# Kernel tuning notes

Measured on AMD Instinct MI355X. Metric: run time of the kernel, lower is better.

Reference implementation:

```python
import jax, jax.numpy as jnp
import numpy as np

N = 4096            # num nodes
D = 256             # feature dim
NUM_SUPER_NODES = 6
THRESHOLD = 0.0
EPS = 1e-10
DENSITY = 0.02      # pre-symmetrization edge density


def setup_inputs() -> dict:
    key = jax.random.key(0)
    kx, ka = jax.random.split(key)
    X = jax.random.normal(kx, (N, D), dtype=jnp.float32)
    U = jax.random.uniform(ka, (N, N), dtype=jnp.float32)
    A = (U < DENSITY).astype(jnp.float32)
    A = jnp.maximum(A, A.T)                      # symmetric 0/1 adjacency
    A = A * (1.0 - jnp.eye(N, dtype=jnp.float32))  # no self-loops
    return {"X": X, "A": A}


def _greedy_labels(sim_np, n, num_super, threshold):
    """Sequential greedy union-find merge over pairs sorted by similarity.
    Matches torch: stable descending sort on sim only; merge until
    n - merged <= num_super; relabel roots in first-occurrence order.
    Inherently sequential/data-dependent -> done in numpy on concrete values
    (the torch original also detaches via .item())."""
    iu, ju = np.triu_indices(n, k=1)
    sims = sim_np[iu, ju]
    keep = sims >= threshold
    iu, ju, sims = iu[keep], ju[keep], sims[keep]
    order = np.argsort(-sims, kind="stable")     # stable desc == list.sort(reverse=True)
    parent = np.arange(n)

    def find(i):
        while parent[i] != i:
            parent[i] = parent[parent[i]]        # path halving
            i = parent[i]
        return i

    merged = 0
    for k in order:
        pi, pj = find(int(iu[k])), find(int(ju[k]))
        if pi != pj:
            parent[pj] = pi
            merged += 1
            if n - merged <= num_super:
                break
    mapping = {}
    labels = np.empty(n, dtype=np.int64)
    nl = 0
    for i in range(n):
        r = find(i)
        if r not in mapping:
            mapping[r] = nl
            nl += 1
        labels[i] = mapping[r]
    return labels, nl


def _build_P(A):
    """Vectorized pairwise Jaccard (replaces O(n^2) python loop) + greedy merge."""
    n = A.shape[0]
    A_bin = (A > 0).astype(jnp.float32)
    deg = A_bin.sum(axis=1)                      # |N(i)|
    inter = A_bin @ A_bin.T                      # [n,n] pairwise |Ni & Nj|
    union = deg[:, None] + deg[None, :] - inter  # |Ni | Nj|
    sim = jnp.where(union > 0, inter / jnp.maximum(union, 1.0), 0.0)
    labels, m = _greedy_labels(np.asarray(sim), n, NUM_SUPER_NODES, THRESHOLD)
    P_prime = jax.nn.one_hot(jnp.asarray(labels), m, dtype=jnp.float32)  # [n, m]
    sizes = P_prime.sum(axis=0)
    return P_prime / jnp.sqrt(sizes + EPS)[None, :]   # P = P' @ diag(1/sqrt(sizes+eps))


def reference(X, A):
    P = _build_P(A)                               # [n, m], m == NUM_SUPER_NODES
    X_coarse = P.T @ X                            # [m, D]
    A_coarse = P.T @ A @ P                        # [m, m]
    return (X_coarse, A_coarse, P)
```

## Files before the change

### kernel.cpp

```cpp
#include <hip/hip_runtime.h>

typedef unsigned long long u64;
typedef unsigned short u16;

#define NN 4096
#define NCH 64
#define NSUP 6

__global__ __launch_bounds__(256) void k_packdeg(const float* __restrict__ A,
                                                 u64* __restrict__ bits,
                                                 u16* __restrict__ deg,
                                                 float* out, int out_n,
                                                 int* comp, int* ncomp, int* mstcnt) {
  int t = threadIdx.x;
  int w = t >> 6, lane = t & 63;
  int row = blockIdx.x * 4 + w;
  const float* rp = A + (size_t)row * NN;
  u64 my = 0;
  int dsum = 0;
#pragma unroll 8
  for (int k = 0; k < 64; ++k) {
    float v = rp[k * 64 + lane];
    u64 m = __ballot(v > 0.0f);
    dsum += __popcll(m);
    if (lane == k) my = m;
  }
  bits[(size_t)row * NCH + lane] = my;
  if (lane == 0) deg[row] = (u16)dsum;
  int g = blockIdx.x * 256 + t;
  if (g < out_n) out[g] = 0.0f;
  if (g < NN) comp[g] = g;
  if (g == 0) { *ncomp = NN; *mstcnt = 0; }
}

__global__ __launch_bounds__(256) void k_inter(const u64* __restrict__ bits,
                                               u16* __restrict__ inter) {
  __shared__ ulonglong2 L[2][64 * 8];
  int b = blockIdx.x;
  int by = (int)((129.0f - sqrtf(16641.0f - 8.0f * (float)b)) * 0.5f) - 1;
  if (by < 0) by = 0;
#define CUM(y) (64 * (y) - ((y) * ((y) - 1)) / 2)
  while (by < 63 && CUM(by + 1) <= b) ++by;
  while (CUM(by) > b) --by;
  int bx = by + (b - CUM(by));
#undef CUM
  int i0 = by * 64, j0 = bx * 64;
  int t = threadIdx.x;
  int tx = t & 15, ty = t >> 4;
  int swA = ty & 7, swB = tx & 7;
  int slotL = t & 7, rowL = t >> 3;
  int sw0 = (rowL >> 2) & 7, sw1 = ((rowL + 32) >> 2) & 7;
  int acc[4][4] = {};
  for (int st = 0; st < 4; ++st) {
    __syncthreads();
    {
      const ulonglong2* gi0 = reinterpret_cast<const ulonglong2*>(bits + (size_t)(i0 + rowL) * NCH);
      const ulonglong2* gi1 = reinterpret_cast<const ulonglong2*>(bits + (size_t)(i0 + rowL + 32) * NCH);
      const ulonglong2* gj0 = reinterpret_cast<const ulonglong2*>(bits + (size_t)(j0 + rowL) * NCH);
      const ulonglong2* gj1 = reinterpret_cast<const ulonglong2*>(bits + (size_t)(j0 + rowL + 32) * NCH);
      L[0][rowL * 8 + (slotL ^ sw0)] = gi0[st * 8 + slotL];
      L[0][(rowL + 32) * 8 + (slotL ^ sw1)] = gi1[st * 8 + slotL];
      L[1][rowL * 8 + (slotL ^ sw0)] = gj0[st * 8 + slotL];
      L[1][(rowL + 32) * 8 + (slotL ^ sw1)] = gj1[st * 8 + slotL];
    }
    __syncthreads();
    for (int s = 0; s < 8; ++s) {
      ulonglong2 av[4], bv[4];
#pragma unroll
      for (int a = 0; a < 4; ++a) av[a] = L[0][(ty * 4 + a) * 8 + (s ^ swA)];
#pragma unroll
      for (int c = 0; c < 4; ++c) bv[c] = L[1][(tx * 4 + c) * 8 + (s ^ swB)];
#pragma unroll
      for (int a = 0; a < 4; ++a)
#pragma unroll
        for (int c = 0; c < 4; ++c)
          acc[a][c] += __popcll(av[a].x & bv[c].x) + __popcll(av[a].y & bv[c].y);
    }
  }
#pragma unroll
  for (int a = 0; a < 4; ++a) {
    int i = i0 + ty * 4 + a;
    ushort4 wv;
    wv.x = (u16)acc[a][0]; wv.y = (u16)acc[a][1];
    wv.z = (u16)acc[a][2]; wv.w = (u16)acc[a][3];
    *reinterpret_cast<ushort4*>(inter + (size_t)i * NN + j0 + tx * 4) = wv;
  }
  if (bx != by) {
#pragma unroll
    for (int c = 0; c < 4; ++c) {
      int j = j0 + tx * 4 + c;
      ushort4 wv;
      wv.x = (u16)acc[0][c]; wv.y = (u16)acc[1][c];
      wv.z = (u16)acc[2][c]; wv.w = (u16)acc[3][c];
      *reinterpret_cast<ushort4*>(inter + (size_t)j * NN + i0 + ty * 4) = wv;
    }
  }
}

__global__ __launch_bounds__(256) void k_scan(const u16* __restrict__ inter,
                                              const u16* __restrict__ deg,
                                              const int* __restrict__ comp,
                                              const int* __restrict__ ncomp,
                                              u64* __restrict__ nkey,
                                              int* __restrict__ nu) {
  if (*ncomp <= 1) return;
  __shared__ u16 comp_s[NN];
  __shared__ u16 deg_s[NN];
  int t = threadIdx.x;
  for (int i = t; i < NN / 8; i += 256) {
    int4 ca = reinterpret_cast<const int4*>(comp)[i * 2];
    int4 cb = reinterpret_cast<const int4*>(comp)[i * 2 + 1];
    uint4 pk;
    pk.x = (unsigned)ca.x | ((unsigned)ca.y << 16);
    pk.y = (unsigned)ca.z | ((unsigned)ca.w << 16);
    pk.z = (unsigned)cb.x | ((unsigned)cb.y << 16);
    pk.w = (unsigned)cb.z | ((unsigned)cb.w << 16);
    reinterpret_cast<uint4*>(comp_s)[i] = pk;
    reinterpret_cast<uint4*>(deg_s)[i] = reinterpret_cast<const uint4*>(deg)[i];
  }
  __syncthreads();
  int w = t >> 6, lane = t & 63;
  int v = blockIdx.x * 4 + w;
  int cv = (int)comp_s[v];
  int dv = (int)deg_s[v];
  const u16* row = inter + (size_t)v * NN;
  u64 key = 0;
  for (int it = 0; it < 8; ++it) {
    int ub = it * 512 + lane * 8;
    uint4 pv = *reinterpret_cast<const uint4*>(row + ub);
    uint4 dg = reinterpret_cast<const uint4*>(deg_s)[ub >> 3];
    uint4 cs = reinterpret_cast<const uint4*>(comp_s)[ub >> 3];
    unsigned pw[4] = { pv.x, pv.y, pv.z, pv.w };
    unsigned dw[4] = { dg.x, dg.y, dg.z, dg.w };
    unsigned cw[4] = { cs.x, cs.y, cs.z, cs.w };
#pragma unroll
    for (int k = 0; k < 8; ++k) {
      int iv = (int)((pw[k >> 1] >> ((k & 1) * 16)) & 0xFFFF);
      int du = (int)((dw[k >> 1] >> ((k & 1) * 16)) & 0xFFFF);
      int cu = (int)((cw[k >> 1] >> ((k & 1) * 16)) & 0xFFFF);
      int un = dv + du - iv;
      float s = (un > 0) ? ((float)iv / (float)un) : 0.0f;
      unsigned sb = __float_as_uint(s);
      u64 kk = (cu != cv)
                   ? (((u64)sb << 32) | (u64)(0xFFFFFFFFu - (unsigned)(ub + k)))
                   : 0ull;
      if (kk > key) key = kk;
    }
  }
#pragma unroll
  for (int off = 32; off > 0; off >>= 1) {
    unsigned lo = (unsigned)key, hi = (unsigned)(key >> 32);
    unsigned olo = __shfl_xor(lo, off, 64), ohi = __shfl_xor(hi, off, 64);
    u64 o = ((u64)ohi << 32) | (u64)olo;
    if (o > key) key = o;
  }
  if (lane == 0) {
    u64 pk = 0; int u = -1;
    if (key != 0ull) {
      unsigned simb = (unsigned)(key >> 32);
      u = (int)(0xFFFFFFFFu - (unsigned)(key & 0xFFFFFFFFull));
      int i = v < u ? v : u, j = v < u ? u : v;
      unsigned idx = (unsigned)i * (unsigned)(2 * NN - i - 1) / 2u + (unsigned)(j - i - 1);
      pk = ((u64)simb << 24) | (u64)(0xFFFFFFu - idx);
    }
    nkey[v] = pk; nu[v] = u;
  }
}

__global__ __launch_bounds__(1024) void k_merge(const u64* __restrict__ nkey,
                                                const int* __restrict__ nu,
                                                int* comp, int* ncomp, int* mstcnt,
                                                u64* mkey, int* mi, int* mj,
                                                int* labels_g, float* invs_g, float* out) {
  if (*ncomp <= 1) return;
  __shared__ int parent_s[NN];
  __shared__ u64 cbest_s[NN];
  __shared__ unsigned char mk_s[NN];
  __shared__ int roots[16];
  __shared__ int rcnt, cnt_s, chg_s, changed;
  __shared__ int szs[8];
  __shared__ float ivs[8];
  int t = threadIdx.x;
  for (int c = t; c < NN; c += 1024) { parent_s[c] = c; cbest_s[c] = 0ull; }
  __syncthreads();
  for (int v = t; v < NN; v += 1024) {
    u64 k = nkey[v];
    if (k) atomicMax(&cbest_s[comp[v]], k);
  }
  __syncthreads();
  for (int v = t; v < NN; v += 1024) {
    u64 k = nkey[v];
    if (!k) continue;
    int c = comp[v];
    if (k == cbest_s[c]) {
      int u = nu[v];
      int cu = comp[u];
      bool mutual = (cbest_s[cu] == k);
      if (!mutual || v < u) {
        int slot = atomicAdd(mstcnt, 1);
        if (slot < 4352) { mkey[slot] = k; mi[slot] = v; mj[slot] = u; }
      }
      parent_s[c] = cu;
    }
  }
  __syncthreads();
  for (int c = t; c < NN; c += 1024) {
    int pc = parent_s[c];
    if (parent_s[pc] == c && c < pc) parent_s[c] = c;
  }
  __syncthreads();
  for (int it = 0; it < 13; ++it) {
    if (t == 0) chg_s = 0;
    __syncthreads();
    for (int c = t; c < NN; c += 1024) {
      int p1 = parent_s[c], p2 = parent_s[p1];
      if (p1 != p2) { parent_s[c] = p2; chg_s = 1; }
    }
    __syncthreads();
    if (!chg_s) break;
  }
  for (int c = t; c < NN; c += 1024) mk_s[c] = 0;
  if (t == 0) cnt_s = 0;
  __syncthreads();
  for (int v = t; v < NN; v += 1024) {
    int nc = parent_s[comp[v]];
    comp[v] = nc;
    mk_s[nc] = 1;
  }
  __syncthreads();
  int lc = 0;
  for (int c = t; c < NN; c += 1024) lc += mk_s[c];
  atomicAdd(&cnt_s, lc);
  __syncthreads();
  if (t == 0) *ncomp = cnt_s;
  __syncthreads();
  if (cnt_s != 1) return;
  int* rr = reinterpret_cast<int*>(cbest_s);
  u64* rk = cbest_s + 2048;
  int* rs = reinterpret_cast<int*>(cbest_s + 3072);
  int nm = *mstcnt;
  if (nm < 0) nm = 0;
  if (nm > 4352) nm = 4352;
  for (int v = t; v < NN; v += 1024) parent_s[v] = v;
  for (int pass = 0; pass < NSUP - 1; ++pass) {
    u64 bk = ~0ull; int bsel = -1;
    for (int e = t; e < nm; e += 1024) { u64 k = mkey[e]; if (k < bk) { bk = k; bsel = e; } }
    rk[t] = bk; rs[t] = bsel;
    __syncthreads();
    for (int s = 512; s > 0; s >>= 1) {
      if (t < s && rk[t + s] < rk[t]) { rk[t] = rk[t + s]; rs[t] = rs[t + s]; }
      __syncthreads();
    }
    if (t == 0 && rs[0] >= 0) mkey[rs[0]] = ~0ull;
    __syncthreads();
  }
  for (int round = 0; round < 64; ++round) {
    if (t == 0) changed = 0;
    __syncthreads();
    for (int e = t; e < nm; e += 1024) {
      if (mkey[e] == ~0ull) continue;
      int a = parent_s[mi[e]], b = parent_s[mj[e]];
      if (a == b) continue;
      int m = a < b ? a : b, M = a < b ? b : a;
      int old = atomicMin(&parent_s[M], m);
      if (old > m) changed = 1;
    }
    __syncthreads();
    for (int rep = 0; rep < 3; ++rep) {
      for (int v = t; v < NN; v += 1024) parent_s[v] = parent_s[parent_s[v]];
      __syncthreads();
    }
    int ch = changed;
    __syncthreads();
    if (!ch) break;
  }
  for (int rep = 0; rep < 13; ++rep) {
    for (int v = t; v < NN; v += 1024) parent_s[v] = parent_s[parent_s[v]];
    __syncthreads();
  }
  if (t == 0) rcnt = 0;
  __syncthreads();
  for (int v = t; v < NN; v += 1024)
    if (parent_s[v] == v) { int s = atomicAdd(&rcnt, 1); if (s < 16) roots[s] = v; }
  __syncthreads();
  if (t == 0) {
    int c = rcnt > 16 ? 16 : rcnt;
    for (int a = 1; a < c; ++a) {
      int x = roots[a]; int b2 = a - 1;
      while (b2 >= 0 && roots[b2] > x) { roots[b2 + 1] = roots[b2]; --b2; }
      roots[b2 + 1] = x;
    }
  }
  if (t < 8) szs[t] = 0;
  __syncthreads();
  if (t < rcnt && t < 16) rr[roots[t]] = t;
  __syncthreads();
  for (int v = t; v < NN; v += 1024) {
    int lab = rr[parent_s[v]];
    labels_g[v] = lab;
    atomicAdd(&szs[lab], 1);
  }
  __syncthreads();
  if (t < rcnt && t < 8) {
    float iv = 1.0f / sqrtf((float)szs[t] + 1e-10f);
    ivs[t] = iv; invs_g[t] = iv;
  }
  __syncthreads();
  for (int v = t; v < NN; v += 1024) {
    int lab = rr[parent_s[v]];
    float* base = out + 1572 + v * 6;
#pragma unroll
    for (int b2 = 0; b2 < 6; ++b2) base[b2] = (b2 == lab) ? ivs[lab] : 0.0f;
  }
}

__global__ __launch_bounds__(256) void k_coarse(const float* __restrict__ X,
                                                const u64* __restrict__ bits,
                                                const int* __restrict__ labels,
                                                const float* __restrict__ invs,
                                                float* out) {
  int t = threadIdx.x;
  if (blockIdx.x < 64) {
    __shared__ float acc[6][256];
    __shared__ int labs[64];
    __shared__ float ivl[64];
#pragma unroll
    for (int m = 0; m < 6; ++m) acc[m][t] = 0.0f;
    if (t < 64) { int v = blockIdx.x * 64 + t; int l = labels[v]; labs[t] = l; ivl[t] = invs[l]; }
    __syncthreads();
    int v0 = blockIdx.x * 64;
    for (int r = 0; r < 64; ++r) {
      float x = X[(size_t)(v0 + r) * 256 + t];
      acc[labs[r]][t] += ivl[r] * x;
    }
    __syncthreads();
#pragma unroll
    for (int m = 0; m < 6; ++m) atomicAdd(&out[m * 256 + t], acc[m][t]);
  } else {
    __shared__ unsigned char labs8[NN];
    __shared__ float accA[36];
    __shared__ float ivsl[8];
    for (int v = t; v < NN; v += 256) labs8[v] = (unsigned char)labels[v];
    if (t < 36) accA[t] = 0.0f;
    if (t < 6) ivsl[t] = invs[t];
    __syncthreads();
    int i = (blockIdx.x - 64) * 256 + t;
    u64 cnt = 0;
    const u64* row = bits + (size_t)i * NCH;
    for (int c = 0; c < NCH; ++c) {
      u64 wm = row[c];
      while (wm) {
        int j = (c << 6) + __builtin_ctzll(wm);
        wm &= wm - 1;
        cnt += 1ull << (labs8[j] * 10);
      }
    }
    int li = labs8[i];
    float fi = ivsl[li];
#pragma unroll
    for (int b = 0; b < 6; ++b) {
      float cb = (float)((cnt >> (b * 10)) & 1023ull);
      if (cb != 0.0f) atomicAdd(&accA[li * 6 + b], fi * ivsl[b] * cb);
    }
    __syncthreads();
    if (t < 36) atomicAdd(&out[1536 + t], accA[t]);
  }
}

extern "C" void kernel_launch(void* const* d_in, const int* in_sizes, int n_in,
                              void* d_out, int out_size, void* d_ws, size_t ws_size,
                              hipStream_t stream) {
  const float* X = (const float*)d_in[0];
  const float* A = (const float*)d_in[1];
  float* out = (float*)d_out;

  char* wp = (char*)d_ws;
  size_t off = 0;
#define WALLOC(ty, name, count) \
  ty* name = (ty*)(wp + off);   \
  off += (((size_t)(count) * sizeof(ty)) + 255) & ~(size_t)255;
  WALLOC(u64, bits, (size_t)NN * NCH)
  WALLOC(u16, inter, (size_t)NN * NN)
  WALLOC(u16, deg, NN)
  WALLOC(int, comp, NN)
  WALLOC(u64, nkey, NN)
  WALLOC(int, nu, NN)
  WALLOC(u64, mkey, 4352)
  WALLOC(int, mi, 4352)
  WALLOC(int, mj, 4352)
  WALLOC(int, labels, NN)
  WALLOC(float, invs, 8)
  WALLOC(int, ncomp, 1)
  WALLOC(int, mstcnt, 1)
#undef WALLOC
  if (off > ws_size) return;

  k_packdeg<<<NN / 4, 256, 0, stream>>>(A, bits, deg, out, out_size, comp, ncomp, mstcnt);
  k_inter<<<2080, 256, 0, stream>>>(bits, inter);
  for (int ph = 0; ph < 12; ++ph) {
    k_scan<<<NN / 4, 256, 0, stream>>>(inter, deg, comp, ncomp, nkey, nu);
    k_merge<<<1, 1024, 0, stream>>>(nkey, nu, comp, ncomp, mstcnt, mkey, mi, mj,
                                    labels, invs, out);
  }
  k_coarse<<<80, 256, 0, stream>>>(X, bits, labels, invs, out);
}
```

Before: 381.9 us.

## Fuse scan and merge into one kernel using last-block completion counter

Merges the per-phase scan kernel and the single-block merge kernel into one launch. The last block to finish, detected with an atomic done counter, performs the Boruvka merge using global cbest and 16-bit shared parent arrays. This removes 12 kernel launches and the serial 1024-thread launch gap each phase, at the cost of running the merge with only 256 threads. The inter kernel is also reworked to load 16 chunks per stage with a different LDS swizzle, halving the number of staging rounds.

```diff
diff --git a/kernel.cpp b/kernel.cpp
--- a/kernel.cpp
+++ b/kernel.cpp
@@ -6,12 +6,14 @@
 #define NN 4096
 #define NCH 64
 #define NSUP 6
+#define NPB 1024
 
 __global__ __launch_bounds__(256) void k_packdeg(const float* __restrict__ A,
                                                  u64* __restrict__ bits,
                                                  u16* __restrict__ deg,
                                                  float* out, int out_n,
-                                                 int* comp, int* ncomp, int* mstcnt) {
+                                                 int* comp, int* ncomp, int* mstcnt,
+                                                 u64* cbest, unsigned* done) {
   int t = threadIdx.x;
   int w = t >> 6, lane = t & 63;
   int row = blockIdx.x * 4 + w;
@@ -29,13 +31,14 @@
   if (lane == 0) deg[row] = (u16)dsum;
   int g = blockIdx.x * 256 + t;
   if (g < out_n) out[g] = 0.0f;
-  if (g < NN) comp[g] = g;
+  if (g < NN) { comp[g] = g; cbest[g] = 0ull; }
+  if (g < 16) done[g] = 0u;
   if (g == 0) { *ncomp = NN; *mstcnt = 0; }
 }
 
 __global__ __launch_bounds__(256) void k_inter(const u64* __restrict__ bits,
                                                u16* __restrict__ inter) {
-  __shared__ ulonglong2 L[2][64 * 8];
+  __shared__ ulonglong2 L[2][64 * 16];
   int b = blockIdx.x;
   int by = (int)((129.0f - sqrtf(16641.0f - 8.0f * (float)b)) * 0.5f) - 1;
   if (by < 0) by = 0;
@@ -47,34 +50,37 @@
   int i0 = by * 64, j0 = bx * 64;
   int t = threadIdx.x;
   int tx = t & 15, ty = t >> 4;
-  int swA = ty & 7, swB = tx & 7;
-  int slotL = t & 7, rowL = t >> 3;
-  int sw0 = (rowL >> 2) & 7, sw1 = ((rowL + 32) >> 2) & 7;
+  int rowA[4], swA[4], rowB[4], swB[4];
+#pragma unroll
+  for (int a = 0; a < 4; ++a) {
+    rowA[a] = ty * 4 + a; swA[a] = (rowA[a] ^ (rowA[a] >> 2)) & 7;
+    rowB[a] = tx * 4 + a; swB[a] = (rowB[a] ^ (rowB[a] >> 2)) & 7;
+  }
+  int cuL = t & 15, rg = t >> 4;
   int acc[4][4] = {};
-  for (int st = 0; st < 4; ++st) {
-    __syncthreads();
-    {
-      const ulonglong2* gi0 = reinterpret_cast<const ulonglong2*>(bits + (size_t)(i0 + rowL) * NCH);
-      const ulonglong2* gi1 = reinterpret_cast<const ulonglong2*>(bits + (size_t)(i0 + rowL + 32) * NCH);
-      const ulonglong2* gj0 = reinterpret_cast<const ulonglong2*>(bits + (size_t)(j0 + rowL) * NCH);
-      const ulonglong2* gj1 = reinterpret_cast<const ulonglong2*>(bits + (size_t)(j0 + rowL + 32) * NCH);
-      L[0][rowL * 8 + (slotL ^ sw0)] = gi0[st * 8 + slotL];
-      L[0][(rowL + 32) * 8 + (slotL ^ sw1)] = gi1[st * 8 + slotL];
-      L[1][rowL * 8 + (slotL ^ sw0)] = gj0[st * 8 + slotL];
-      L[1][(rowL + 32) * 8 + (slotL ^ sw1)] = gj1[st * 8 + slotL];
-    }
-    __syncthreads();
-    for (int s = 0; s < 8; ++s) {
+  for (int st = 0; st < 2; ++st) {
+    __syncthreads();
+#pragma unroll
+    for (int rr = 0; rr < 4; ++rr) {
+      int row = rg * 4 + rr;
+      int sw = (row ^ (row >> 2)) & 7;
+      L[0][row * 16 + (cuL ^ sw)] =
+          reinterpret_cast<const ulonglong2*>(bits + (size_t)(i0 + row) * NCH)[st * 16 + cuL];
+      L[1][row * 16 + (cuL ^ sw)] =
+          reinterpret_cast<const ulonglong2*>(bits + (size_t)(j0 + row) * NCH)[st * 16 + cuL];
+    }
+    __syncthreads();
+    for (int cu = 0; cu < 16; ++cu) {
       ulonglong2 av[4], bv[4];
 #pragma unroll
-      for (int a = 0; a < 4; ++a) av[a] = L[0][(ty * 4 + a) * 8 + (s ^ swA)];
-#pragma unroll
-      for (int c = 0; c < 4; ++c) bv[c] = L[1][(tx * 4 + c) * 8 + (s ^ swB)];
+      for (int a = 0; a < 4; ++a) av[a] = L[0][rowA[a] * 16 + (cu ^ swA[a])];
+#pragma unroll
+      for (int b2 = 0; b2 < 4; ++b2) bv[b2] = L[1][rowB[b2] * 16 + (cu ^ swB[b2])];
 #pragma unroll
       for (int a = 0; a < 4; ++a)
 #pragma unroll
-        for (int c = 0; c < 4; ++c)
-          acc[a][c] += __popcll(av[a].x & bv[c].x) + __popcll(av[a].y & bv[c].y);
+        for (int b2 = 0; b2 < 4; ++b2)
+          acc[a][b2] += __popcll(av[a].x & bv[b2].x) + __popcll(av[a].y & bv[b2].y);
     }
   }
 #pragma unroll
@@ -87,25 +93,32 @@
   }
   if (bx != by) {
 #pragma unroll
-    for (int c = 0; c < 4; ++c) {
-      int j = j0 + tx * 4 + c;
+    for (int b2 = 0; b2 < 4; ++b2) {
+      int j = j0 + tx * 4 + b2;
       ushort4 wv;
-      wv.x = (u16)acc[0][c]; wv.y = (u16)acc[1][c];
-      wv.z = (u16)acc[2][c]; wv.w = (u16)acc[3][c];
+      wv.x = (u16)acc[0][b2]; wv.y = (u16)acc[1][b2];
+      wv.z = (u16)acc[2][b2]; wv.w = (u16)acc[3][b2];
       *reinterpret_cast<ushort4*>(inter + (size_t)j * NN + i0 + ty * 4) = wv;
     }
   }
 }
 
-__global__ __launch_bounds__(256) void k_scan(const u16* __restrict__ inter,
-                                              const u16* __restrict__ deg,
-                                              const int* __restrict__ comp,
-                                              const int* __restrict__ ncomp,
-                                              u64* __restrict__ nkey,
-                                              int* __restrict__ nu) {
+__global__ __launch_bounds__(256) void k_phase(const u16* __restrict__ inter,
+                                               const u16* __restrict__ deg,
+                                               int* comp, int* ncomp, int* mstcnt,
+                                               u64* __restrict__ nkey, int* __restrict__ nu,
+                                               u64* mkey, int* mi, int* mj,
+                                               u64* cbest, unsigned* done, int ph,
+                                               int* labels_g, float* invs_g, float* out) {
   if (*ncomp <= 1) return;
   __shared__ u16 comp_s[NN];
   __shared__ u16 deg_s[NN];
+  __shared__ u64 rk[256];
+  __shared__ int rs[256];
+  __shared__ int roots[16];
+  __shared__ int rcnt, cnt_s, chg_s, changed, amLast;
+  __shared__ int szs[8];
+  __shared__ float ivs[8];
   int t = threadIdx.x;
   for (int i = t; i < NN / 8; i += 256) {
     int4 ca = reinterpret_cast<const int4*>(comp)[i * 2];
@@ -119,135 +132,136 @@
     reinterpret_cast<uint4*>(deg_s)[i] = reinterpret_cast<const uint4*>(deg)[i];
   }
   __syncthreads();
-  int w = t >> 6, lane = t & 63;
-  int v = blockIdx.x * 4 + w;
-  int cv = (int)comp_s[v];
-  int dv = (int)deg_s[v];
-  const u16* row = inter + (size_t)v * NN;
-  u64 key = 0;
-  for (int it = 0; it < 8; ++it) {
-    int ub = it * 512 + lane * 8;
-    uint4 pv = *reinterpret_cast<const uint4*>(row + ub);
-    uint4 dg = reinterpret_cast<const uint4*>(deg_s)[ub >> 3];
-    uint4 cs = reinterpret_cast<const uint4*>(comp_s)[ub >> 3];
-    unsigned pw[4] = { pv.x, pv.y, pv.z, pv.w };
-    unsigned dw[4] = { dg.x, dg.y, dg.z, dg.w };
-    unsigned cw[4] = { cs.x, cs.y, cs.z, cs.w };
-#pragma unroll
-    for (int k = 0; k < 8; ++k) {
-      int iv = (int)((pw[k >> 1] >> ((k & 1) * 16)) & 0xFFFF);
-      int du = (int)((dw[k >> 1] >> ((k & 1) * 16)) & 0xFFFF);
-      int cu = (int)((cw[k >> 1] >> ((k & 1) * 16)) & 0xFFFF);
-      int un = dv + du - iv;
-      float s = (un > 0) ? ((float)iv / (float)un) : 0.0f;
-      unsigned sb = __float_as_uint(s);
-      u64 kk = (cu != cv)
-                   ? (((u64)sb << 32) | (u64)(0xFFFFFFFFu - (unsigned)(ub + k)))
-                   : 0ull;
-      if (kk > key) key = kk;
-    }
-  }
-#pragma unroll
-  for (int off = 32; off > 0; off >>= 1) {
-    unsigned lo = (unsigned)key, hi = (unsigned)(key >> 32);
-    unsigned olo = __shfl_xor(lo, off, 64), ohi = __shfl_xor(hi, off, 64);
-    u64 o = ((u64)ohi << 32) | (u64)olo;
-    if (o > key) key = o;
-  }
-  if (lane == 0) {
-    u64 pk = 0; int u = -1;
-    if (key != 0ull) {
-      unsigned simb = (unsigned)(key >> 32);
-      u = (int)(0xFFFFFFFFu - (unsigned)(key & 0xFFFFFFFFull));
-      int i = v < u ? v : u, j = v < u ? u : v;
-      unsigned idx = (unsigned)i * (unsigned)(2 * NN - i - 1) / 2u + (unsigned)(j - i - 1);
-      pk = ((u64)simb << 24) | (u64)(0xFFFFFFu - idx);
-    }
-    nkey[v] = pk; nu[v] = u;
-  }
-}
-
-__global__ __launch_bounds__(1024) void k_merge(const u64* __restrict__ nkey,
-                                                const int* __restrict__ nu,
-                                                int* comp, int* ncomp, int* mstcnt,
-                                                u64* mkey, int* mi, int* mj,
-                                                int* labels_g, float* invs_g, float* out) {
-  if (*ncomp <= 1) return;
-  __shared__ int parent_s[NN];
-  __shared__ u64 cbest_s[NN];
-  __shared__ unsigned char mk_s[NN];
-  __shared__ int roots[16];
-  __shared__ int rcnt, cnt_s, chg_s, changed;
-  __shared__ int szs[8];
-  __shared__ float ivs[8];
-  int t = threadIdx.x;
-  for (int c = t; c < NN; c += 1024) { parent_s[c] = c; cbest_s[c] = 0ull; }
-  __syncthreads();
-  for (int v = t; v < NN; v += 1024) {
+  {
+    int w = t >> 6, lane = t & 63;
+    int v = blockIdx.x * 4 + w;
+    int cv = (int)comp_s[v];
+    int dv = (int)deg_s[v];
+    const u16* row = inter + (size_t)v * NN;
+    u64 key = 0;
+    for (int it = 0; it < 8; ++it) {
+      int ub = it * 512 + lane * 8;
+      uint4 pv = *reinterpret_cast<const uint4*>(row + ub);
+      uint4 dg = reinterpret_cast<const uint4*>(deg_s)[ub >> 3];
+      uint4 cs = reinterpret_cast<const uint4*>(comp_s)[ub >> 3];
+      unsigned pw[4] = { pv.x, pv.y, pv.z, pv.w };
+      unsigned dw[4] = { dg.x, dg.y, dg.z, dg.w };
+      unsigned cw[4] = { cs.x, cs.y, cs.z, cs.w };
+#pragma unroll
+      for (int k = 0; k < 8; ++k) {
+        int iv = (int)((pw[k >> 1] >> ((k & 1) * 16)) & 0xFFFF);
+        int du = (int)((dw[k >> 1] >> ((k & 1) * 16)) & 0xFFFF);
+        int cu = (int)((cw[k >> 1] >> ((k & 1) * 16)) & 0xFFFF);
+        int un = dv + du - iv;
+        float s = (un > 0) ? ((float)iv / (float)un) : 0.0f;
+        unsigned sb = __float_as_uint(s);
+        u64 kk = (cu != cv)
+                     ? (((u64)sb << 32) | (u64)(0xFFFFFFFFu - (unsigned)(ub + k)))
+                     : 0ull;
+        if (kk > key) key = kk;
+      }
+    }
+#pragma unroll
+    for (int off = 32; off > 0; off >>= 1) {
+      unsigned lo = (unsigned)key, hi = (unsigned)(key >> 32);
+      unsigned olo = __shfl_xor(lo, off, 64), ohi = __shfl_xor(hi, off, 64);
+      u64 o = ((u64)ohi << 32) | (u64)olo;
+      if (o > key) key = o;
+    }
+    if (lane == 0) {
+      u64 pk = 0; int u = -1;
+      if (key != 0ull) {
+        unsigned simb = (unsigned)(key >> 32);
+        u = (int)(0xFFFFFFFFu - (unsigned)(key & 0xFFFFFFFFull));
+        int i = v < u ? v : u, j = v < u ? u : v;
+        unsigned idx = (unsigned)i * (unsigned)(2 * NN - i - 1) / 2u + (unsigned)(j - i - 1);
+        pk = ((u64)simb << 24) | (u64)(0xFFFFFFu - idx);
+      }
+      nkey[v] = pk; nu[v] = u;
+    }
+  }
+  __threadfence();
+  __syncthreads();
+  if (t == 0) {
+    unsigned old = __hip_atomic_fetch_add(done + ph, 1u, __ATOMIC_ACQ_REL,
+                                          __HIP_MEMORY_SCOPE_AGENT);
+    amLast = (old == (unsigned)(NPB - 1));
+  }
+  __syncthreads();
+  if (!amLast) return;
+  __threadfence();
+  u16* parent16 = deg_s;
+  u64* markbits = rk;
+  for (int v = t; v < NN; v += 256) {
     u64 k = nkey[v];
-    if (k) atomicMax(&cbest_s[comp[v]], k);
-  }
-  __syncthreads();
-  for (int v = t; v < NN; v += 1024) {
+    if (k) atomicMax(&cbest[(int)comp_s[v]], k);
+  }
+  __syncthreads();
+  __threadfence();
+  for (int c = t; c < NN; c += 256) parent16[c] = (u16)c;
+  __syncthreads();
+  for (int v = t; v < NN; v += 256) {
     u64 k = nkey[v];
     if (!k) continue;
-    int c = comp[v];
-    if (k == cbest_s[c]) {
+    int c = (int)comp_s[v];
+    u64 cb = __hip_atomic_load(&cbest[c], __ATOMIC_RELAXED, __HIP_MEMORY_SCOPE_AGENT);
+    if (k == cb) {
       int u = nu[v];
-      int cu = comp[u];
-      bool mutual = (cbest_s[cu] == k);
+      int cu = (int)comp_s[u];
+      u64 cbu = __hip_atomic_load(&cbest[cu], __ATOMIC_RELAXED, __HIP_MEMORY_SCOPE_AGENT);
+      bool mutual = (cbu == k);
       if (!mutual || v < u) {
         int slot = atomicAdd(mstcnt, 1);
         if (slot < 4352) { mkey[slot] = k; mi[slot] = v; mj[slot] = u; }
       }
-      parent_s[c] = cu;
-    }
-  }
-  __syncthreads();
-  for (int c = t; c < NN; c += 1024) {
-    int pc = parent_s[c];
-    if (parent_s[pc] == c && c < pc) parent_s[c] = c;
+      parent16[c] = (u16)cu;
+    }
+  }
+  __syncthreads();
+  for (int c = t; c < NN; c += 256) {
+    int pc = (int)parent16[c];
+    if ((int)parent16[pc] == c && c < pc) parent16[c] = (u16)c;
   }
   __syncthreads();
   for (int it = 0; it < 13; ++it) {
     if (t == 0) chg_s = 0;
     __syncthreads();
-    for (int c = t; c < NN; c += 1024) {
-      int p1 = parent_s[c], p2 = parent_s[p1];
-      if (p1 != p2) { parent_s[c] = p2; chg_s = 1; }
+    for (int c = t; c < NN; c += 256) {
+      int p1 = (int)parent16[c], p2 = (int)parent16[p1];
+      if (p1 != p2) { parent16[c] = (u16)p2; chg_s = 1; }
     }
     __syncthreads();
     if (!chg_s) break;
   }
-  for (int c = t; c < NN; c += 1024) mk_s[c] = 0;
+  if (t < 64) markbits[t] = 0ull;
   if (t == 0) cnt_s = 0;
   __syncthreads();
-  for (int v = t; v < NN; v += 1024) {
-    int nc = parent_s[comp[v]];
+  for (int v = t; v < NN; v += 256) {
+    int nc = (int)parent16[(int)comp_s[v]];
     comp[v] = nc;
-    mk_s[nc] = 1;
-  }
-  __syncthreads();
-  int lc = 0;
-  for (int c = t; c < NN; c += 1024) lc += mk_s[c];
-  atomicAdd(&cnt_s, lc);
+    atomicOr(&markbits[nc >> 6], 1ull << (nc & 63));
+  }
+  __syncthreads();
+  if (t < 64) atomicAdd(&cnt_s, __popcll(markbits[t]));
   __syncthreads();
   if (t == 0) *ncomp = cnt_s;
+  for (int c = t; c < NN; c += 256)
+    __hip_atomic_store(&cbest[c], 0ull, __ATOMIC_RELAXED, __HIP_MEMORY_SCOPE_AGENT);
   __syncthreads();
   if (cnt_s != 1) return;
-  int* rr = reinterpret_cast<int*>(cbest_s);
-  u64* rk = cbest_s + 2048;
-  int* rs = reinterpret_cast<int*>(cbest_s + 3072);
+  u16* p16 = comp_s;
+  u16* rr16 = deg_s;
   int nm = *mstcnt;
   if (nm < 0) nm = 0;
   if (nm > 4352) nm = 4352;
-  for (int v = t; v < NN; v += 1024) parent_s[v] = v;
+  for (int v = t; v < NN; v += 256) p16[v] = (u16)v;
+  __syncthreads();
   for (int pass = 0; pass < NSUP - 1; ++pass) {
     u64 bk = ~0ull; int bsel = -1;
-    for (int e = t; e < nm; e += 1024) { u64 k = mkey[e]; if (k < bk) { bk = k; bsel = e; } }
+    for (int e = t; e < nm; e += 256) { u64 k = mkey[e]; if (k < bk) { bk = k; bsel = e; } }
     rk[t] = bk; rs[t] = bsel;
     __syncthreads();
-    for (int s = 512; s > 0; s >>= 1) {
+    for (int s = 128; s > 0; s >>= 1) {
       if (t < s && rk[t + s] < rk[t]) { rk[t] = rk[t + s]; rs[t] = rs[t + s]; }
       __syncthreads();
     }
@@ -257,17 +271,16 @@
   for (int round = 0; round < 64; ++round) {
     if (t == 0) changed = 0;
     __syncthreads();
-    for (int e = t; e < nm; e += 1024) {
+    for (int e = t; e < nm; e += 256) {
       if (mkey[e] == ~0ull) continue;
-      int a = parent_s[mi[e]], b = parent_s[mj[e]];
+      int a = (int)p16[mi[e]], b = (int)p16[mj[e]];
       if (a == b) continue;
       int m = a < b ? a : b, M = a < b ? b : a;
-      int old = atomicMin(&parent_s[M], m);
-      if (old > m) changed = 1;
+      if ((int)p16[M] > m) { p16[M] = (u16)m; changed = 1; }
     }
     __syncthreads();
     for (int rep = 0; rep < 3; ++rep) {
-      for (int v = t; v < NN; v += 1024) parent_s[v] = parent_s[parent_s[v]];
+      for (int v = t; v < NN; v += 256) p16[v] = p16[(int)p16[v]];
       __syncthreads();
     }
     int ch = changed;
@@ -275,13 +288,13 @@
     if (!ch) break;
   }
   for (int rep = 0; rep < 13; ++rep) {
-    for (int v = t; v < NN; v += 1024) parent_s[v] = parent_s[parent_s[v]];
+    for (int v = t; v < NN; v += 256) p16[v] = p16[(int)p16[v]];
     __syncthreads();
   }
   if (t == 0) rcnt = 0;
   __syncthreads();
-  for (int v = t; v < NN; v += 1024)
-    if (parent_s[v] == v) { int s = atomicAdd(&rcnt, 1); if (s < 16) roots[s] = v; }
+  for (int v = t; v < NN; v += 256)
+    if ((int)p16[v] == v) { int s = atomicAdd(&rcnt, 1); if (s < 16) roots[s] = v; }
   __syncthreads();
   if (t == 0) {
     int c = rcnt > 16 ? 16 : rcnt;
@@ -293,10 +306,10 @@
   }
   if (t < 8) szs[t] = 0;
   __syncthreads();
-  if (t < rcnt && t < 16) rr[roots[t]] = t;
-  __syncthreads();
-  for (int v = t; v < NN; v += 1024) {
-    int lab = rr[parent_s[v]];
+  if (t < rcnt && t < 16) rr16[roots[t]] = (u16)t;
+  __syncthreads();
+  for (int v = t; v < NN; v += 256) {
+    int lab = (int)rr16[(int)p16[v]];
     labels_g[v] = lab;
     atomicAdd(&szs[lab], 1);
   }
@@ -306,8 +319,8 @@
     ivs[t] = iv; invs_g[t] = iv;
   }
   __syncthreads();
-  for (int v = t; v < NN; v += 1024) {
-    int lab = rr[parent_s[v]];
+  for (int v = t; v < NN; v += 256) {
+    int lab = (int)rr16[(int)p16[v]];
     float* base = out + 1572 + v * 6;
 #pragma unroll
     for (int b2 = 0; b2 < 6; ++b2) base[b2] = (b2 == lab) ? ivs[lab] : 0.0f;
@@ -388,19 +401,21 @@
   WALLOC(u64, mkey, 4352)
   WALLOC(int, mi, 4352)
   WALLOC(int, mj, 4352)
+  WALLOC(u64, cbest, NN)
   WALLOC(int, labels, NN)
   WALLOC(float, invs, 8)
   WALLOC(int, ncomp, 1)
   WALLOC(int, mstcnt, 1)
+  WALLOC(unsigned, done, 16)
 #undef WALLOC
   if (off > ws_size) return;
 
-  k_packdeg<<<NN / 4, 256, 0, stream>>>(A, bits, deg, out, out_size, comp, ncomp, mstcnt);
+  k_packdeg<<<NN / 4, 256, 0, stream>>>(A, bits, deg, out, out_size, comp, ncomp, mstcnt,
+                                        cbest, done);
   k_inter<<<2080, 256, 0, stream>>>(bits, inter);
   for (int ph = 0; ph < 12; ++ph) {
-    k_scan<<<NN / 4, 256, 0, stream>>>(inter, deg, comp, ncomp, nkey, nu);
-    k_merge<<<1, 1024, 0, stream>>>(nkey, nu, comp, ncomp, mstcnt, mkey, mi, mj,
-                                    labels, invs, out);
+    k_phase<<<NPB, 256, 0, stream>>>(inter, deg, comp, ncomp, mstcnt, nkey, nu,
+                                     mkey, mi, mj, cbest, done, ph, labels, invs, out);
   }
   k_coarse<<<80, 256, 0, stream>>>(X, bits, labels, invs, out);
 }
```

New measurement: 937.7 us. +145.5%, slower.
